# Kernel tuning notes

Measured on AMD Instinct MI355X. Metric: run time of the kernel, lower is better.

Reference implementation:

```python
import jax, jax.numpy as jnp
import numpy as np

B, T, C = 4, 2048, 1024
H, D = 16, 64

def setup_inputs() -> dict:
    key = jax.random.key(0)
    k1, k2, k3 = jax.random.split(key, 3)
    x = jax.random.normal(k1, (B, T, C), dtype=jnp.float32)
    Wqkv = jax.random.normal(k2, (C, 3 * C), dtype=jnp.float32) * (1.0 / np.sqrt(C))
    Wproj = jax.random.normal(k3, (C, C), dtype=jnp.float32) * (1.0 / np.sqrt(C))
    return {"x": x, "Wqkv": Wqkv, "Wproj": Wproj}

def reference(x, Wqkv, Wproj):
    Bx, Tx, Cx = x.shape
    qkv = x @ Wqkv                       # (B, T, 3C)
    q, k, v = jnp.split(qkv, 3, axis=-1)
    # (B, T, C) -> (B, H, T, D)
    q = q.reshape(Bx, Tx, H, D).transpose(0, 2, 1, 3)
    k = k.reshape(Bx, Tx, H, D).transpose(0, 2, 1, 3)
    v = v.reshape(Bx, Tx, H, D).transpose(0, 2, 1, 3)
    att = jnp.einsum('bhqd,bhkd->bhqk', q, k) / jnp.sqrt(jnp.float32(D))
    causal = jnp.tril(jnp.ones((Tx, Tx), dtype=bool))  # (T, T)
    att = jnp.where(causal[None, None, :, :], att, jnp.float32(-jnp.inf))
    att = jax.nn.softmax(att, axis=-1)
    y = jnp.einsum('bhqk,bhkd->bhqd', att, v)          # (B, H, T, D)
    y = y.transpose(0, 2, 1, 3).reshape(Bx, Tx, Cx)
    return y @ Wproj
```

## Files before the change

### kernel.cpp

```cpp
#include <hip/hip_runtime.h>
#include <cstdint>
#include <cstddef>


typedef short bf16x8 __attribute__((ext_vector_type(8)));
typedef float f32x4 __attribute__((ext_vector_type(4)));

#define MFMA32(a, b, c) __builtin_amdgcn_mfma_f32_16x16x32_bf16((a), (b), (c), 0, 0, 0)

__device__ __forceinline__ unsigned short f2b(float f) {
  unsigned int x = __builtin_bit_cast(unsigned int, f);
  x += 0x7fffu + ((x >> 16) & 1u);
  return (unsigned short)(x >> 16);
}

__device__ __forceinline__ unsigned int pack2(float a, float b) {
  return (unsigned int)f2b(a) | ((unsigned int)f2b(b) << 16);
}

__device__ __forceinline__ unsigned int cvtpk(float a, float b) {
  unsigned int r;
  asm("v_cvt_pk_bf16_f32 %0, %1, %2" : "=v"(r) : "v"(a), "v"(b));
  return r;
}

__device__ __forceinline__ float exp2v(float x) {
  float r;
  asm("v_exp_f32 %0, %1" : "=v"(r) : "v"(x));
  return r;
}

__device__ __forceinline__ void gload16(const void* g, void* l) {
  __builtin_amdgcn_global_load_lds(
      (const __attribute__((address_space(1))) void*)g,
      (__attribute__((address_space(3))) void*)l, 16, 0, 0);
}

__global__ __launch_bounds__(256) void k_conv_x(const float* __restrict__ in,
                                                unsigned short* __restrict__ out, int n4) {
  int i = blockIdx.x * 256 + threadIdx.x;
  if (i >= n4) return;
  float4 v = reinterpret_cast<const float4*>(in)[i];
  ushort4 o;
  o.x = f2b(v.x); o.y = f2b(v.y); o.z = f2b(v.z); o.w = f2b(v.w);
  reinterpret_cast<ushort4*>(out)[i] = o;
}

__global__ __launch_bounds__(256) void k_transpose(const float* __restrict__ in,
                                                   unsigned short* __restrict__ out,
                                                   int R, int C) {
  __shared__ float tile[32][33];
  int c0 = blockIdx.x * 32, r0 = blockIdx.y * 32;
  int tx = threadIdx.x & 31, ty = threadIdx.x >> 5;
#pragma unroll
  for (int j = 0; j < 4; ++j)
    tile[ty + 8 * j][tx] = in[(size_t)(r0 + ty + 8 * j) * C + c0 + tx];
  __syncthreads();
#pragma unroll
  for (int j = 0; j < 4; ++j)
    out[(size_t)(c0 + ty + 8 * j) * R + r0 + tx] = f2b(tile[tx][ty + 8 * j]);
}

template <int EPI>
__global__ __launch_bounds__(256) void k_gemm(const unsigned short* __restrict__ A,
                                              const unsigned short* __restrict__ Bt,
                                              float* __restrict__ outF,
                                              unsigned short* __restrict__ q_ws,
                                              unsigned short* __restrict__ k_ws,
                                              unsigned short* __restrict__ v_ws,
                                              int M, int N) {
  constexpr int K = 1024;
  __shared__ unsigned short smem[16384];
  unsigned short* As = smem;
  unsigned short* Bs = smem + 8192;
  const int bn = blockIdx.x, bm = blockIdx.y;
  const int tid = threadIdx.x;
  const int w = tid >> 6, lane = tid & 63;
  const int wm = w >> 1, wn = w & 1;
  const int c = lane & 15, g = lane >> 4;

  f32x4 acc[4][4];
#pragma unroll
  for (int i = 0; i < 4; ++i)
#pragma unroll
    for (int j = 0; j < 4; ++j) acc[i][j] = (f32x4){0.f, 0.f, 0.f, 0.f};

  const int srow = 32 * w + (lane >> 3);
  const int scol = 8 * (lane & 7);
  const unsigned short* Ag = A + (size_t)(bm * 128 + srow) * K + scol;
  const unsigned short* Bg = Bt + (size_t)(bn * 128 + srow) * K + scol;
  char* AsB = (char*)As + w * 4096;
  char* BsB = (char*)Bs + w * 4096;

  for (int kt = 0; kt < K / 64; ++kt) {
    const int kb = kt * 64;
    __syncthreads();
#pragma unroll
    for (int i = 0; i < 4; ++i) {
      gload16(Ag + (size_t)(8 * i) * K + kb, AsB + i * 1024);
      gload16(Bg + (size_t)(8 * i) * K + kb, BsB + i * 1024);
    }
    asm volatile("s_waitcnt vmcnt(0)" ::: "memory");
    __syncthreads();
#pragma unroll
    for (int u = 0; u < 2; ++u) {
      bf16x8 af[4], bfr[4];
#pragma unroll
      for (int mf = 0; mf < 4; ++mf)
        af[mf] = *(const bf16x8*)((const char*)As + (wm * 64 + mf * 16 + c) * 128 + u * 64 + g * 16);
#pragma unroll
      for (int nf = 0; nf < 4; ++nf)
        bfr[nf] = *(const bf16x8*)((const char*)Bs + (wn * 64 + nf * 16 + c) * 128 + u * 64 + g * 16);
#pragma unroll
      for (int mf = 0; mf < 4; ++mf)
#pragma unroll
        for (int nf = 0; nf < 4; ++nf)
          acc[mf][nf] = MFMA32(af[mf], bfr[nf], acc[mf][nf]);
    }
  }

  const int rowb = bm * 128 + wm * 64;
  const int colb = bn * 128 + wn * 64;
  if (EPI == 1) {
#pragma unroll
    for (int mf = 0; mf < 4; ++mf)
#pragma unroll
      for (int nf = 0; nf < 4; ++nf)
#pragma unroll
        for (int r = 0; r < 4; ++r) {
          int row = rowb + mf * 16 + 4 * g + r;
          int col = colb + nf * 16 + c;
          outF[(size_t)row * N + col] = acc[mf][nf][r];
        }
  } else {
    const int sec = colb >> 10;
    const int hh = (colb & 1023) >> 6;
    const int b = rowb >> 11, t0 = rowb & 2047;
    unsigned short* Lw = smem + w * 4096;

    __syncthreads();
    if (sec < 2) {
      const float sc = (sec == 0) ? 0.125f * 1.4426950408889634f : 1.f;
#pragma unroll
      for (int mf = 0; mf < 4; ++mf)
#pragma unroll
        for (int nf = 0; nf < 4; ++nf)
#pragma unroll
          for (int r = 0; r < 4; ++r)
            Lw[(16 * mf + 4 * g + r) * 64 + 16 * nf + c] = f2b(acc[mf][nf][r] * sc);
    } else {
#pragma unroll
      for (int mf = 0; mf < 4; ++mf)
#pragma unroll
        for (int nf = 0; nf < 4; ++nf)
#pragma unroll
          for (int rr = 0; rr < 2; ++rr)
            *(unsigned int*)&Lw[(16 * nf + c) * 64 + 16 * mf + 4 * g + 2 * rr] =
                pack2(acc[mf][nf][2 * rr], acc[mf][nf][2 * rr + 1]);
    }
    asm volatile("s_waitcnt lgkmcnt(0)" ::: "memory");
    const int rw = lane >> 3, ch = lane & 7;
    const int chx = ch ^ rw;
    if (sec == 0) {
      unsigned short* dst = q_ws + ((size_t)(b * 16 + hh) * 2048 + t0) * 64;
#pragma unroll
      for (int i = 0; i < 8; ++i) {
        int tl = i * 8 + rw;
        *(bf16x8*)(dst + (size_t)tl * 64 + ch * 8) = *(const bf16x8*)&Lw[tl * 64 + ch * 8];
      }
    } else if (sec == 1) {
      unsigned short* dst = k_ws + ((size_t)(b * 16 + hh) * 2048 + t0) * 64;
#pragma unroll
      for (int i = 0; i < 8; ++i) {
        int tl = i * 8 + rw;
        *(bf16x8*)(dst + (size_t)tl * 64 + chx * 8) = *(const bf16x8*)&Lw[tl * 64 + ch * 8];
      }
    } else {
      unsigned short* dst = v_ws + (size_t)(b * 16 + hh) * 64 * 2048 + t0;
#pragma unroll
      for (int i = 0; i < 8; ++i) {
        int dl = i * 8 + rw;
        *(bf16x8*)(dst + (size_t)dl * 2048 + chx * 8) = *(const bf16x8*)&Lw[dl * 64 + ch * 8];
      }
    }
  }
}

__global__ __launch_bounds__(512) void k_attn(const unsigned short* __restrict__ q_ws,
                                              const unsigned short* __restrict__ k_ws,
                                              const unsigned short* __restrict__ v_ws,
                                              unsigned short* __restrict__ y_ws) {
  constexpr int T = 2048;
  __shared__ unsigned short Ks[2][64 * 64];
  __shared__ unsigned short Vs[2][64 * 64];
  const int f = blockIdx.x;
  const int f2 = (f & 7) * 64 + (f >> 3);
  const int bh = f2 >> 3;
  const int xi = f2 & 7;
  const int tid = threadIdx.x, w = tid >> 6, lane = tid & 63;
  const int c = lane & 15, g = lane >> 4;
  const int cl = c & 7;
  const size_t base = (size_t)bh * T * 64;
  const unsigned short* Kb = k_ws + base;
  const unsigned short* Vb = v_ws + base;
  const unsigned short* Qb = q_ws + base;

  const int srow = w * 8 + (lane >> 3);
  const int sch = lane & 7;

#pragma unroll 1
  for (int ph = 0; ph < 2; ++ph) {
    const int q0 = (ph == 0 ? xi : 15 - xi) * 128;
    const int qrow = q0 + 16 * w + c;
    const int q_max_wave = q0 + 16 * w + 15;
    const int n_kt = (q0 >> 6) + 2;
    bf16x8 qf[2];
#pragma unroll
    for (int u = 0; u < 2; ++u)
      qf[u] = *(const bf16x8*)(Qb + (size_t)qrow * 64 + 32 * u + 8 * g);

    f32x4 yacc[4];
#pragma unroll
    for (int i = 0; i < 4; ++i) yacc[i] = (f32x4){0.f, 0.f, 0.f, 0.f};
    float m_run = -1e30f, l_part = 0.f;

    __syncthreads();
    gload16(Kb + (size_t)srow * 64 + sch * 8, (char*)&Ks[0][0] + w * 1024);
    gload16(Vb + (size_t)srow * T + sch * 8, (char*)&Vs[0][0] + w * 1024);

#pragma unroll 1
    for (int kt = 0; kt < n_kt; ++kt) {
      const int k0 = kt * 64;
      const int cur = kt & 1;
      if (kt + 1 < n_kt) {
        const int k0n = k0 + 64;
        gload16(Kb + (size_t)(k0n + srow) * 64 + sch * 8, (char*)&Ks[cur ^ 1][0] + w * 1024);
        gload16(Vb + (size_t)srow * T + k0n + sch * 8, (char*)&Vs[cur ^ 1][0] + w * 1024);
        asm volatile("s_waitcnt vmcnt(2)" ::: "memory");
      } else {
        asm volatile("s_waitcnt vmcnt(0)" ::: "memory");
      }
      __builtin_amdgcn_s_barrier();

      if (k0 <= q_max_wave) {
        const char* KsC = (const char*)&Ks[cur][0];
        const char* VsC = (const char*)&Vs[cur][0];
        f32x4 s[4];
        __builtin_amdgcn_s_setprio(1);
#pragma unroll
        for (int tf = 0; tf < 4; ++tf) {
          bf16x8 kf0 = *(const bf16x8*)(KsC + (16 * tf + c) * 128 + (g ^ cl) * 16);
          bf16x8 kf1 = *(const bf16x8*)(KsC + (16 * tf + c) * 128 + ((4 + g) ^ cl) * 16);
          f32x4 z = (f32x4){0.f, 0.f, 0.f, 0.f};
          z = MFMA32(kf0, qf[0], z);
          s[tf] = MFMA32(kf1, qf[1], z);
        }
        __builtin_amdgcn_s_setprio(0);
        if (k0 + 63 > q0 + 16 * w) {
#pragma unroll
          for (int tf = 0; tf < 4; ++tf)
#pragma unroll
            for (int r = 0; r < 4; ++r)
              if (k0 + 16 * tf + 4 * g + r > qrow) s[tf][r] = -1e30f;
        }
        float mx0 = fmaxf(fmaxf(s[0][0], s[0][1]), fmaxf(s[0][2], s[0][3]));
        float mx1 = fmaxf(fmaxf(s[1][0], s[1][1]), fmaxf(s[1][2], s[1][3]));
        float mx2 = fmaxf(fmaxf(s[2][0], s[2][1]), fmaxf(s[2][2], s[2][3]));
        float mx3 = fmaxf(fmaxf(s[3][0], s[3][1]), fmaxf(s[3][2], s[3][3]));
        float mx = fmaxf(fmaxf(mx0, mx1), fmaxf(mx2, mx3));
        mx = fmaxf(mx, __shfl_xor(mx, 16));
        mx = fmaxf(mx, __shfl_xor(mx, 32));
        if (__any(mx > m_run + 11.5f)) {
          float m_new = fmaxf(m_run, mx);
          float corr = exp2v(m_run - m_new);
          l_part *= corr;
#pragma unroll
          for (int i = 0; i < 4; ++i) yacc[i] *= corr;
          m_run = m_new;
        }
        float p[16];
#pragma unroll
        for (int tf = 0; tf < 4; ++tf)
#pragma unroll
          for (int r = 0; r < 4; ++r) p[tf * 4 + r] = exp2v(s[tf][r] - m_run);
        float ps = ((p[0] + p[1]) + (p[2] + p[3])) + ((p[4] + p[5]) + (p[6] + p[7]));
        ps += ((p[8] + p[9]) + (p[10] + p[11])) + ((p[12] + p[13]) + (p[14] + p[15]));
        l_part += ps;

#pragma unroll
        for (int h = 0; h < 2; ++h) {
          unsigned int lo0 = cvtpk(p[8 * h + 0], p[8 * h + 1]);
          unsigned int hi0 = cvtpk(p[8 * h + 2], p[8 * h + 3]);
          unsigned int lo1 = cvtpk(p[8 * h + 4], p[8 * h + 5]);
          unsigned int hi1 = cvtpk(p[8 * h + 6], p[8 * h + 7]);
          int a2 = 2 * (g & 1);
          int srcA = 16 * a2 + c, srcB = srcA + 16;
          unsigned int Al0 = __shfl(lo0, srcA), Ah0 = __shfl(hi0, srcA);
          unsigned int Al1 = __shfl(lo1, srcA), Ah1 = __shfl(hi1, srcA);
          unsigned int Bl0 = __shfl(lo0, srcB), Bh0 = __shfl(hi0, srcB);
          unsigned int Bl1 = __shfl(lo1, srcB), Bh1 = __shfl(hi1, srcB);
          bool f1 = (g >= 2);
          union { unsigned int u[4]; bf16x8 v; } pf;
          pf.u[0] = f1 ? Al1 : Al0;
          pf.u[1] = f1 ? Ah1 : Ah0;
          pf.u[2] = f1 ? Bl1 : Bl0;
          pf.u[3] = f1 ? Bh1 : Bh0;
          __builtin_amdgcn_s_setprio(1);
#pragma unroll
          for (int df = 0; df < 4; ++df) {
            bf16x8 vf = *(const bf16x8*)(VsC + (16 * df + c) * 128 + ((h * 4 + g) ^ cl) * 16);
            yacc[df] = MFMA32(vf, pf.v, yacc[df]);
          }
          __builtin_amdgcn_s_setprio(0);
        }
      }
      __builtin_amdgcn_s_barrier();
    }

    float lt = l_part;
    lt += __shfl_xor(lt, 16);
    lt += __shfl_xor(lt, 32);
    float inv = 1.f / lt;
    const int b = bh >> 4, hh = bh & 15;
#pragma unroll
    for (int df = 0; df < 4; ++df) {
      uint2 o;
      o.x = cvtpk(yacc[df][0] * inv, yacc[df][1] * inv);
      o.y = cvtpk(yacc[df][2] * inv, yacc[df][3] * inv);
      *(uint2*)(y_ws + (size_t)(b * 2048 + qrow) * 1024 + hh * 64 + 16 * df + 4 * g) = o;
    }
  }
}

extern "C" void kernel_launch(void* const* d_in, const int* in_sizes, int n_in,
                              void* d_out, int out_size, void* d_ws, size_t ws_size,
                              hipStream_t stream) {
  const float* x = (const float*)d_in[0];
  const float* Wqkv = (const float*)d_in[1];
  const float* Wproj = (const float*)d_in[2];
  float* out = (float*)d_out;
  char* ws = (char*)d_ws;

  unsigned short* x_bf = (unsigned short*)(ws);
  unsigned short* wqkvT = (unsigned short*)(ws + 16777216);
  unsigned short* wprojT = (unsigned short*)(ws + 23068672);
  unsigned short* q_ws = (unsigned short*)(ws + 25165824);
  unsigned short* k_ws = (unsigned short*)(ws + 41943040);
  unsigned short* v_ws = (unsigned short*)(ws + 58720256);
  unsigned short* y_ws = (unsigned short*)(ws + 75497472);

  k_conv_x<<<8192, 256, 0, stream>>>(x, x_bf, 2097152);
  k_transpose<<<dim3(96, 32), 256, 0, stream>>>(Wqkv, wqkvT, 1024, 3072);
  k_transpose<<<dim3(32, 32), 256, 0, stream>>>(Wproj, wprojT, 1024, 1024);
  k_gemm<0><<<dim3(24, 64), 256, 0, stream>>>(x_bf, wqkvT, nullptr, q_ws, k_ws, v_ws, 8192, 3072);
  k_attn<<<512, 512, 0, stream>>>(q_ws, k_ws, v_ws, y_ws);
  k_gemm<1><<<dim3(8, 64), 256, 0, stream>>>(y_ws, wprojT, out, nullptr, nullptr, nullptr, 8192, 1024);
}
```

Measured before the change: 196.8 us.

## Process two 16-row query groups per wave in attention to reuse K/V fragments

Each wave now handles 32 query rows (two 16-row groups) instead of 16, so each block covers 256 query rows and the grid halves to 256 blocks. K and V fragments read from LDS are reused across both row groups, which halves LDS traffic and global K/V loads per query row. In exchange, register pressure roughly doubles for accumulators and probabilities. The causal diagonal work is coarser, and the half-size grid gives fewer blocks to spread across the CUs, which may hurt occupancy and load balance.

```diff
diff --git a/kernel.cpp b/kernel.cpp
--- a/kernel.cpp
+++ b/kernel.cpp
@@ -194,9 +194,9 @@
   __shared__ unsigned short Ks[2][64 * 64];
   __shared__ unsigned short Vs[2][64 * 64];
   const int f = blockIdx.x;
-  const int f2 = (f & 7) * 64 + (f >> 3);
-  const int bh = f2 >> 3;
-  const int xi = f2 & 7;
+  const int f2 = (f & 7) * 32 + (f >> 3);
+  const int bh = f2 >> 2;
+  const int xi = f2 & 3;
   const int tid = threadIdx.x, w = tid >> 6, lane = tid & 63;
   const int c = lane & 15, g = lane >> 4;
   const int cl = c & 7;
@@ -210,19 +210,24 @@
 
 #pragma unroll 1
   for (int ph = 0; ph < 2; ++ph) {
-    const int q0 = (ph == 0 ? xi : 15 - xi) * 128;
-    const int qrow = q0 + 16 * w + c;
-    const int q_max_wave = q0 + 16 * w + 15;
-    const int n_kt = (q0 >> 6) + 2;
-    bf16x8 qf[2];
-#pragma unroll
-    for (int u = 0; u < 2; ++u)
-      qf[u] = *(const bf16x8*)(Qb + (size_t)qrow * 64 + 32 * u + 8 * g);
-
-    f32x4 yacc[4];
-#pragma unroll
-    for (int i = 0; i < 4; ++i) yacc[i] = (f32x4){0.f, 0.f, 0.f, 0.f};
-    float m_run = -1e30f, l_part = 0.f;
+    const int q0 = (ph == 0 ? xi : 7 - xi) * 256;
+    const int qb = q0 + 32 * w;
+    const int qrow0 = qb + c;
+    const int qrow1 = qb + 16 + c;
+    const int n_kt = (q0 >> 6) + 4;
+    bf16x8 qf0[2], qf1[2];
+#pragma unroll
+    for (int u = 0; u < 2; ++u) {
+      qf0[u] = *(const bf16x8*)(Qb + (size_t)qrow0 * 64 + 32 * u + 8 * g);
+      qf1[u] = *(const bf16x8*)(Qb + (size_t)qrow1 * 64 + 32 * u + 8 * g);
+    }
+
+    f32x4 yacc[2][4];
+#pragma unroll
+    for (int rg = 0; rg < 2; ++rg)
+#pragma unroll
+      for (int i = 0; i < 4; ++i) yacc[rg][i] = (f32x4){0.f, 0.f, 0.f, 0.f};
+    float m0 = -1e30f, m1 = -1e30f, l0 = 0.f, l1 = 0.f;
 
     __syncthreads();
     gload16(Kb + (size_t)srow * 64 + sch * 8, (char*)&Ks[0][0] + w * 1024);
@@ -242,74 +247,109 @@
       }
       __builtin_amdgcn_s_barrier();
 
-      if (k0 <= q_max_wave) {
+      if (k0 <= qb + 31) {
         const char* KsC = (const char*)&Ks[cur][0];
         const char* VsC = (const char*)&Vs[cur][0];
-        f32x4 s[4];
+        f32x4 s0[4], s1[4];
         __builtin_amdgcn_s_setprio(1);
 #pragma unroll
         for (int tf = 0; tf < 4; ++tf) {
           bf16x8 kf0 = *(const bf16x8*)(KsC + (16 * tf + c) * 128 + (g ^ cl) * 16);
           bf16x8 kf1 = *(const bf16x8*)(KsC + (16 * tf + c) * 128 + ((4 + g) ^ cl) * 16);
           f32x4 z = (f32x4){0.f, 0.f, 0.f, 0.f};
-          z = MFMA32(kf0, qf[0], z);
-          s[tf] = MFMA32(kf1, qf[1], z);
+          z = MFMA32(kf0, qf0[0], z);
+          s0[tf] = MFMA32(kf1, qf0[1], z);
+          f32x4 z2 = (f32x4){0.f, 0.f, 0.f, 0.f};
+          z2 = MFMA32(kf0, qf1[0], z2);
+          s1[tf] = MFMA32(kf1, qf1[1], z2);
         }
         __builtin_amdgcn_s_setprio(0);
-        if (k0 + 63 > q0 + 16 * w) {
+        if (k0 + 63 > qb) {
 #pragma unroll
           for (int tf = 0; tf < 4; ++tf)
 #pragma unroll
             for (int r = 0; r < 4; ++r)
-              if (k0 + 16 * tf + 4 * g + r > qrow) s[tf][r] = -1e30f;
-        }
-        float mx0 = fmaxf(fmaxf(s[0][0], s[0][1]), fmaxf(s[0][2], s[0][3]));
-        float mx1 = fmaxf(fmaxf(s[1][0], s[1][1]), fmaxf(s[1][2], s[1][3]));
-        float mx2 = fmaxf(fmaxf(s[2][0], s[2][1]), fmaxf(s[2][2], s[2][3]));
-        float mx3 = fmaxf(fmaxf(s[3][0], s[3][1]), fmaxf(s[3][2], s[3][3]));
-        float mx = fmaxf(fmaxf(mx0, mx1), fmaxf(mx2, mx3));
-        mx = fmaxf(mx, __shfl_xor(mx, 16));
-        mx = fmaxf(mx, __shfl_xor(mx, 32));
-        if (__any(mx > m_run + 11.5f)) {
-          float m_new = fmaxf(m_run, mx);
-          float corr = exp2v(m_run - m_new);
-          l_part *= corr;
-#pragma unroll
-          for (int i = 0; i < 4; ++i) yacc[i] *= corr;
-          m_run = m_new;
-        }
-        float p[16];
+              if (k0 + 16 * tf + 4 * g + r > qrow0) s0[tf][r] = -1e30f;
+        }
+        if (k0 + 63 > qb + 16) {
+#pragma unroll
+          for (int tf = 0; tf < 4; ++tf)
+#pragma unroll
+            for (int r = 0; r < 4; ++r)
+              if (k0 + 16 * tf + 4 * g + r > qrow1) s1[tf][r] = -1e30f;
+        }
+        float mxa = -1e30f, mxb = -1e30f;
+#pragma unroll
+        for (int tf = 0; tf < 4; ++tf) {
+          mxa = fmaxf(mxa, fmaxf(fmaxf(s0[tf][0], s0[tf][1]), fmaxf(s0[tf][2], s0[tf][3])));
+          mxb = fmaxf(mxb, fmaxf(fmaxf(s1[tf][0], s1[tf][1]), fmaxf(s1[tf][2], s1[tf][3])));
+        }
+        mxa = fmaxf(mxa, __shfl_xor(mxa, 16));
+        mxa = fmaxf(mxa, __shfl_xor(mxa, 32));
+        mxb = fmaxf(mxb, __shfl_xor(mxb, 16));
+        mxb = fmaxf(mxb, __shfl_xor(mxb, 32));
+        if (__any(fmaxf(mxa - m0, mxb - m1) > 11.5f)) {
+          float mn0 = fmaxf(m0, mxa), mn1 = fmaxf(m1, mxb);
+          float c0 = exp2v(m0 - mn0), c1 = exp2v(m1 - mn1);
+          l0 *= c0; l1 *= c1;
+#pragma unroll
+          for (int i = 0; i < 4; ++i) { yacc[0][i] *= c0; yacc[1][i] *= c1; }
+          m0 = mn0; m1 = mn1;
+        }
+        float p0[16], p1[16];
 #pragma unroll
         for (int tf = 0; tf < 4; ++tf)
 #pragma unroll
-          for (int r = 0; r < 4; ++r) p[tf * 4 + r] = exp2v(s[tf][r] - m_run);
-        float ps = ((p[0] + p[1]) + (p[2] + p[3])) + ((p[4] + p[5]) + (p[6] + p[7]));
-        ps += ((p[8] + p[9]) + (p[10] + p[11])) + ((p[12] + p[13]) + (p[14] + p[15]));
-        l_part += ps;
-
+          for (int r = 0; r < 4; ++r) {
+            p0[tf * 4 + r] = exp2v(s0[tf][r] - m0);
+            p1[tf * 4 + r] = exp2v(s1[tf][r] - m1);
+          }
+        float psa = ((p0[0] + p0[1]) + (p0[2] + p0[3])) + ((p0[4] + p0[5]) + (p0[6] + p0[7]));
+        psa += ((p0[8] + p0[9]) + (p0[10] + p0[11])) + ((p0[12] + p0[13]) + (p0[14] + p0[15]));
+        float psb = ((p1[0] + p1[1]) + (p1[2] + p1[3])) + ((p1[4] + p1[5]) + (p1[6] + p1[7]));
+        psb += ((p1[8] + p1[9]) + (p1[10] + p1[11])) + ((p1[12] + p1[13]) + (p1[14] + p1[15]));
+        l0 += psa; l1 += psb;
+
+        const int a2 = 2 * (g & 1);
+        const int srcA = 16 * a2 + c, srcB = srcA + 16;
+        const bool f1 = (g >= 2);
 #pragma unroll
         for (int h = 0; h < 2; ++h) {
-          unsigned int lo0 = cvtpk(p[8 * h + 0], p[8 * h + 1]);
-          unsigned int hi0 = cvtpk(p[8 * h + 2], p[8 * h + 3]);
-          unsigned int lo1 = cvtpk(p[8 * h + 4], p[8 * h + 5]);
-          unsigned int hi1 = cvtpk(p[8 * h + 6], p[8 * h + 7]);
-          int a2 = 2 * (g & 1);
-          int srcA = 16 * a2 + c, srcB = srcA + 16;
-          unsigned int Al0 = __shfl(lo0, srcA), Ah0 = __shfl(hi0, srcA);
-          unsigned int Al1 = __shfl(lo1, srcA), Ah1 = __shfl(hi1, srcA);
-          unsigned int Bl0 = __shfl(lo0, srcB), Bh0 = __shfl(hi0, srcB);
-          unsigned int Bl1 = __shfl(lo1, srcB), Bh1 = __shfl(hi1, srcB);
-          bool f1 = (g >= 2);
-          union { unsigned int u[4]; bf16x8 v; } pf;
-          pf.u[0] = f1 ? Al1 : Al0;
-          pf.u[1] = f1 ? Ah1 : Ah0;
-          pf.u[2] = f1 ? Bl1 : Bl0;
-          pf.u[3] = f1 ? Bh1 : Bh0;
+          union { unsigned int u[4]; bf16x8 v; } pfa, pfb;
+          {
+            unsigned int lo0 = cvtpk(p0[8 * h + 0], p0[8 * h + 1]);
+            unsigned int hi0 = cvtpk(p0[8 * h + 2], p0[8 * h + 3]);
+            unsigned int lo1 = cvtpk(p0[8 * h + 4], p0[8 * h + 5]);
+            unsigned int hi1 = cvtpk(p0[8 * h + 6], p0[8 * h + 7]);
+            unsigned int Al0 = __shfl(lo0, srcA), Ah0 = __shfl(hi0, srcA);
+            unsigned int Al1 = __shfl(lo1, srcA), Ah1 = __shfl(hi1, srcA);
+            unsigned int Bl0 = __shfl(lo0, srcB), Bh0 = __shfl(hi0, srcB);
+            unsigned int Bl1 = __shfl(lo1, srcB), Bh1 = __shfl(hi1, srcB);
+            pfa.u[0] = f1 ? Al1 : Al0;
+            pfa.u[1] = f1 ? Ah1 : Ah0;
+            pfa.u[2] = f1 ? Bl1 : Bl0;
+            pfa.u[3] = f1 ? Bh1 : Bh0;
+          }
+          {
+            unsigned int lo0 = cvtpk(p1[8 * h + 0], p1[8 * h + 1]);
+            unsigned int hi0 = cvtpk(p1[8 * h + 2], p1[8 * h + 3]);
+            unsigned int lo1 = cvtpk(p1[8 * h + 4], p1[8 * h + 5]);
+            unsigned int hi1 = cvtpk(p1[8 * h + 6], p1[8 * h + 7]);
+            unsigned int Al0 = __shfl(lo0, srcA), Ah0 = __shfl(hi0, srcA);
+            unsigned int Al1 = __shfl(lo1, srcA), Ah1 = __shfl(hi1, srcA);
+            unsigned int Bl0 = __shfl(lo0, srcB), Bh0 = __shfl(hi0, srcB);
+            unsigned int Bl1 = __shfl(lo1, srcB), Bh1 = __shfl(hi1, srcB);
+            pfb.u[0] = f1 ? Al1 : Al0;
+            pfb.u[1] = f1 ? Ah1 : Ah0;
+            pfb.u[2] = f1 ? Bl1 : Bl0;
+            pfb.u[3] = f1 ? Bh1 : Bh0;
+          }
           __builtin_amdgcn_s_setprio(1);
 #pragma unroll
           for (int df = 0; df < 4; ++df) {
             bf16x8 vf = *(const bf16x8*)(VsC + (16 * df + c) * 128 + ((h * 4 + g) ^ cl) * 16);
-            yacc[df] = MFMA32(vf, pf.v, yacc[df]);
+            yacc[0][df] = MFMA32(vf, pfa.v, yacc[0][df]);
+            yacc[1][df] = MFMA32(vf, pfb.v, yacc[1][df]);
           }
           __builtin_amdgcn_s_setprio(0);
         }
@@ -317,17 +357,22 @@
       __builtin_amdgcn_s_barrier();
     }
 
-    float lt = l_part;
-    lt += __shfl_xor(lt, 16);
-    lt += __shfl_xor(lt, 32);
-    float inv = 1.f / lt;
     const int b = bh >> 4, hh = bh & 15;
+    float lta = l0, ltb = l1;
+    lta += __shfl_xor(lta, 16);
+    lta += __shfl_xor(lta, 32);
+    ltb += __shfl_xor(ltb, 16);
+    ltb += __shfl_xor(ltb, 32);
+    float inva = 1.f / lta, invb = 1.f / ltb;
 #pragma unroll
     for (int df = 0; df < 4; ++df) {
-      uint2 o;
-      o.x = cvtpk(yacc[df][0] * inv, yacc[df][1] * inv);
-      o.y = cvtpk(yacc[df][2] * inv, yacc[df][3] * inv);
-      *(uint2*)(y_ws + (size_t)(b * 2048 + qrow) * 1024 + hh * 64 + 16 * df + 4 * g) = o;
+      uint2 oa, ob;
+      oa.x = cvtpk(yacc[0][df][0] * inva, yacc[0][df][1] * inva);
+      oa.y = cvtpk(yacc[0][df][2] * inva, yacc[0][df][3] * inva);
+      ob.x = cvtpk(yacc[1][df][0] * invb, yacc[1][df][1] * invb);
+      ob.y = cvtpk(yacc[1][df][2] * invb, yacc[1][df][3] * invb);
+      *(uint2*)(y_ws + (size_t)(b * 2048 + qrow0) * 1024 + hh * 64 + 16 * df + 4 * g) = oa;
+      *(uint2*)(y_ws + (size_t)(b * 2048 + qrow1) * 1024 + hh * 64 + 16 * df + 4 * g) = ob;
     }
   }
 }
@@ -353,6 +398,6 @@
   k_transpose<<<dim3(96, 32), 256, 0, stream>>>(Wqkv, wqkvT, 1024, 3072);
   k_transpose<<<dim3(32, 32), 256, 0, stream>>>(Wproj, wprojT, 1024, 1024);
   k_gemm<0><<<dim3(24, 64), 256, 0, stream>>>(x_bf, wqkvT, nullptr, q_ws, k_ws, v_ws, 8192, 3072);
-  k_attn<<<512, 512, 0, stream>>>(q_ws, k_ws, v_ws, y_ws);
+  k_attn<<<256, 512, 0, stream>>>(q_ws, k_ws, v_ws, y_ws);
   k_gemm<1><<<dim3(8, 64), 256, 0, stream>>>(y_ws, wprojT, out, nullptr, nullptr, nullptr, 8192, 1024);
 }
```

Measured after the change: 206.8 us. 5.1% more time.
